# Kernel tuning notes

Hardware: AMD Instinct MI355X
Metric: run time of the kernel (lower is better)

Reference implementation:

```python
import jax, jax.numpy as jnp
import numpy as np
from jax import lax

EPS = 1e-5
T, N, E = 10, 10000, 320000
C_IN, C_HID, C_OUT = 16, 32, 16


def _stgcn_layer(x, edge_index, edge_weight, tw, tb, gw, gb, gamma, beta):
    # x: [T, N, Cin] -> temporal conv over T per node
    xc = jnp.transpose(x, (1, 2, 0))  # [N, Cin, T]
    y = lax.conv_general_dilated(xc, tw, window_strides=(1,), padding=((1, 1),),
                                 dimension_numbers=("NCH", "OIH", "NCH"))
    y = y + tb[None, :, None]
    y = jnp.clip(y, -10.0, 10.0)
    # InstanceNorm1d (affine, biased var over time axis)
    mu = jnp.mean(y, axis=-1, keepdims=True)
    var = jnp.mean((y - mu) ** 2, axis=-1, keepdims=True)
    y = (y - mu) * lax.rsqrt(var + EPS) * gamma[None, :, None] + beta[None, :, None]
    y = jax.nn.relu(y)
    h = jnp.transpose(y, (0, 2, 1))  # [N, T, C]

    n = h.shape[0]
    # GCNConv normalization (identical at every timestep -> computed once)
    ewn = jax.nn.softmax(edge_weight)  # softmax over all E edges
    loop = jnp.arange(n, dtype=edge_index.dtype)
    row = jnp.concatenate([edge_index[0], loop])  # sources (+self loops)
    col = jnp.concatenate([edge_index[1], loop])  # destinations
    w = jnp.concatenate([ewn, jnp.ones((n,), dtype=ewn.dtype)])
    deg = jax.ops.segment_sum(w, col, num_segments=n)
    dinv = jnp.where(deg > 0, lax.rsqrt(jnp.maximum(deg, EPS * 0 + 1e-30)), 0.0)
    norm = dinv[row] * w * dinv[col]  # [E+N]

    hw = jnp.einsum("ntc,cd->ntd", h, gw)  # [N, T, C]
    msg = hw[row] * norm[:, None, None]     # [E+N, T, C] gather
    agg = jax.ops.segment_sum(msg, col, num_segments=n) + gb  # scatter-add
    out = jnp.clip(jax.nn.relu(agg), -10.0, 10.0)
    return jnp.transpose(out, (1, 0, 2))  # [T, N, C]


def setup_inputs() -> dict:
    key = jax.random.key(0)
    ks = jax.random.split(key, 16)
    inp = {
        "x": jax.random.normal(ks[0], (T, N, C_IN), dtype=jnp.float32),
        "edge_index": jax.random.randint(ks[1], (2, E), 0, N, dtype=jnp.int32),
        "edge_weight": jax.random.uniform(ks[2], (E,), dtype=jnp.float32),
        # layer 1 (in -> hid)
        "l1_tw": jax.random.normal(ks[3], (C_HID, C_IN, 3), dtype=jnp.float32) * 0.02,
        "l1_tb": jnp.zeros((C_HID,), dtype=jnp.float32),
        "l1_gw": jax.random.normal(ks[4], (C_HID, C_HID), dtype=jnp.float32) * 0.1,
        "l1_gb": jnp.zeros((C_HID,), dtype=jnp.float32),
        "l1_gamma": jnp.ones((C_HID,), dtype=jnp.float32),
        "l1_beta": jnp.zeros((C_HID,), dtype=jnp.float32),
        # layer 2 (hid -> hid)
        "l2_tw": jax.random.normal(ks[5], (C_HID, C_HID, 3), dtype=jnp.float32) * 0.02,
        "l2_tb": jnp.zeros((C_HID,), dtype=jnp.float32),
        "l2_gw": jax.random.normal(ks[6], (C_HID, C_HID), dtype=jnp.float32) * 0.1,
        "l2_gb": jnp.zeros((C_HID,), dtype=jnp.float32),
        "l2_gamma": jnp.ones((C_HID,), dtype=jnp.float32),
        "l2_beta": jnp.zeros((C_HID,), dtype=jnp.float32),
        # output linear
        "out_w": jax.random.normal(ks[7], (C_HID, C_OUT), dtype=jnp.float32) * 0.1,
        "out_b": jnp.zeros((C_OUT,), dtype=jnp.float32),
    }
    return inp


def reference(x, edge_index, edge_weight,
              l1_tw, l1_tb, l1_gw, l1_gb, l1_gamma, l1_beta,
              l2_tw, l2_tb, l2_gw, l2_gb, l2_gamma, l2_beta,
              out_w, out_b):
    h = _stgcn_layer(x, edge_index, edge_weight, l1_tw, l1_tb, l1_gw, l1_gb, l1_gamma, l1_beta)
    h = _stgcn_layer(h, edge_index, edge_weight, l2_tw, l2_tb, l2_gw, l2_gb, l2_gamma, l2_beta)
    # per-timestep linear then mean over time == mean then linear, done faithfully
    outs = jnp.einsum("tnc,cd->tnd", h, out_w) + out_b
    return jnp.mean(outs, axis=0)  # [N, C_OUT]
```

## Files before the change

kernel.cpp:

```cpp
#include <hip/hip_runtime.h>
#include <hip/hip_bf16.h>
#include <string.h>


typedef __hip_bfloat16 bf16;

#define TSTEPS 10
#define TPAD 12
#define CHID 32
#define ROWELE (TSTEPS * CHID)
#define ROWW4 40

__device__ __forceinline__ float b2f(bf16 v) { return __bfloat162float(v); }
__device__ __forceinline__ float ldf(const void* p, long i, int bf) {
    return bf ? __bfloat162float(((const bf16*)p)[i]) : ((const float*)p)[i];
}
__device__ __forceinline__ int detect_bf(const unsigned* gbits) {
    return (gbits[0] != 0x3F800000u) ? 1 : 0;
}
__device__ __forceinline__ float bflo(unsigned u) { return __uint_as_float(u << 16); }
__device__ __forceinline__ float bfhi(unsigned u) { return __uint_as_float(u & 0xFFFF0000u); }
__device__ __forceinline__ unsigned pack2bf(float a, float b) {
    bf16 x = __float2bfloat16(a), y = __float2bfloat16(b);
    unsigned short ux, uy;
    memcpy(&ux, &x, 2); memcpy(&uy, &y, 2);
    return (unsigned)ux | ((unsigned)uy << 16);
}
__device__ __forceinline__ unsigned short bfbits(float a) {
    bf16 x = __float2bfloat16(a);
    unsigned short u; memcpy(&u, &x, 2);
    return u;
}
__device__ __forceinline__ void accum8(float* f, uint4 u, float w) {
    f[0] += w * bflo(u.x); f[1] += w * bfhi(u.x);
    f[2] += w * bflo(u.y); f[3] += w * bfhi(u.y);
    f[4] += w * bflo(u.z); f[5] += w * bfhi(u.z);
    f[6] += w * bflo(u.w); f[7] += w * bfhi(u.w);
}


__global__ __launch_bounds__(256) void edge_pass_kernel(
    const void* __restrict__ ew, const unsigned* __restrict__ gbits,
    const int* __restrict__ ei,
    float* __restrict__ ewn, float* __restrict__ degx, int* __restrict__ cnt,
    float* sumexp, int E) {
    int bf = detect_bf(gbits);
    int i0 = (blockIdx.x * 256 + threadIdx.x) * 4;
    float e0 = 0.0f, e1 = 0.0f, e2 = 0.0f, e3 = 0.0f;
    if ((E & 3) == 0 && i0 + 3 < E) {
        float w0, w1, w2, w3;
        if (bf) {
            uint2 u = ((const uint2*)ew)[i0 >> 2];
            w0 = bflo(u.x); w1 = bfhi(u.x); w2 = bflo(u.y); w3 = bfhi(u.y);
        } else {
            float4 f = ((const float4*)ew)[i0 >> 2];
            w0 = f.x; w1 = f.y; w2 = f.z; w3 = f.w;
        }
        e0 = __expf(w0); e1 = __expf(w1); e2 = __expf(w2); e3 = __expf(w3);
        int4 c4 = *(const int4*)&ei[E + i0];
        atomicAdd(&degx[c4.x], e0); atomicAdd(&cnt[c4.x], 1);
        atomicAdd(&degx[c4.y], e1); atomicAdd(&cnt[c4.y], 1);
        atomicAdd(&degx[c4.z], e2); atomicAdd(&cnt[c4.z], 1);
        atomicAdd(&degx[c4.w], e3); atomicAdd(&cnt[c4.w], 1);
        *(float4*)&ewn[i0] = make_float4(e0, e1, e2, e3);
    } else {
        float es[4] = {0, 0, 0, 0};
        for (int j = 0; j < 4; j++) {
            int i = i0 + j;
            if (i < E) {
                float e = __expf(ldf(ew, i, bf));
                es[j] = e;
                ewn[i] = e;
                int c = ei[E + i];
                atomicAdd(&degx[c], e);
                atomicAdd(&cnt[c], 1);
            }
        }
        e0 = es[0]; e1 = es[1]; e2 = es[2]; e3 = es[3];
    }
    float v = (e0 + e1) + (e2 + e3);
    for (int o = 32; o > 0; o >>= 1) v += __shfl_down(v, o);
    __shared__ float s[4];
    int lane = threadIdx.x & 63, wv = threadIdx.x >> 6;
    if (lane == 0) s[wv] = v;
    __syncthreads();
    if (threadIdx.x == 0) atomicAdd(sumexp, s[0] + s[1] + s[2] + s[3]);
}

__global__ __launch_bounds__(1024) void scan_kernel(const int* __restrict__ cnt,
                                                    const float* __restrict__ degx,
                                                    const float* __restrict__ sumexp,
                                                    float* __restrict__ dinv,
                                                    int* __restrict__ off, int N) {
    __shared__ int s[1024];
    int tid = threadIdx.x;
    float invS = 1.0f / (*sumexp);
    for (int i = tid; i < N; i += 1024) dinv[i] = rsqrtf(1.0f + degx[i] * invS);
    int chunk = (N + 1023) / 1024;
    int b0 = tid * chunk;
    int p = 0;
    for (int k = 0; k < chunk; k++) { int i = b0 + k; if (i < N) p += cnt[i]; }
    s[tid] = p;
    __syncthreads();
    for (int d = 1; d < 1024; d <<= 1) {
        int v = (tid >= d) ? s[tid - d] : 0;
        __syncthreads();
        s[tid] += v;
        __syncthreads();
    }
    int base = s[tid] - p;
    for (int k = 0; k < chunk; k++) {
        int i = b0 + k;
        if (i < N) {
            off[i] = base;
            base += cnt[i];
            if (i == N - 1) off[N] = base;
        }
    }
}


__global__ __launch_bounds__(256) void fill_kernel(const int* __restrict__ ei,
                                                   const float* __restrict__ ewn,
                                                   const float* __restrict__ dinv,
                                                   const float* __restrict__ sumexp,
                                                   const int* __restrict__ off,
                                                   int* __restrict__ cursor,
                                                   int2* __restrict__ csr, int E) {
    int i0 = (blockIdx.x * 256 + threadIdx.x) * 4;
    if (i0 >= E) return;
    float invS = 1.0f / (*sumexp);
    if ((E & 3) == 0 && i0 + 3 < E) {
        int4 r4 = *(const int4*)&ei[i0];
        int4 c4 = *(const int4*)&ei[E + i0];
        float4 e4 = *(const float4*)&ewn[i0];
        int rr[4] = {r4.x, r4.y, r4.z, r4.w};
        int cc[4] = {c4.x, c4.y, c4.z, c4.w};
        float ee[4] = {e4.x, e4.y, e4.z, e4.w};
#pragma unroll
        for (int j = 0; j < 4; j++) {
            int r = rr[j], c = cc[j];
            int p = atomicAdd(&cursor[c], 1);
            float w = dinv[r] * (ee[j] * invS) * dinv[c];
            csr[off[c] + p] = make_int2(r, __float_as_int(w));
        }
    } else {
        for (int j = 0; j < 4; j++) {
            int i = i0 + j;
            if (i >= E) break;
            int r = ei[i], c = ei[E + i];
            int p = atomicAdd(&cursor[c], 1);
            float w = dinv[r] * (ewn[i] * invS) * dinv[c];
            csr[off[c] + p] = make_int2(r, __float_as_int(w));
        }
    }
}


template <int CIN, int LAYOUT>
__global__ __launch_bounds__(256) void conv_kernel(
    const void* __restrict__ in_, const unsigned* __restrict__ gbits,
    const void* __restrict__ tw, const void* __restrict__ tb,
    const void* __restrict__ gamma, const void* __restrict__ beta,
    const void* __restrict__ gw,
    bf16* __restrict__ hw, int N) {
    constexpr int CO = CHID;
    __shared__ __align__(16) float s_in[8 * CIN * TPAD];
    __shared__ __align__(16) float s_h[8 * CO * TPAD];
    __shared__ __align__(16) unsigned s_tw01[CIN * CO];
    __shared__ __align__(16) unsigned short s_tw2[CIN * CO];
    __shared__ __align__(16) unsigned s_gwp[(CO / 2) * CO];

    int bfw = detect_bf(gbits);
    int tid = threadIdx.x;
    int nl = tid >> 5, o = tid & 31;

    float tbv = ldf(tb, o, bfw);
    float gav = ldf(gamma, o, bfw);
    float bev = ldf(beta, o, bfw);

    for (int i = tid; i < CIN * CO; i += 256) {
        int ci = i / CO, oo = i % CO;
        long base = ((long)oo * CIN + ci) * 3;
        float w0 = ldf(tw, base, bfw);
        float w1 = ldf(tw, base + 1, bfw);
        float w2 = ldf(tw, base + 2, bfw);
        s_tw01[ci * CO + oo] = pack2bf(w0, w1);
        s_tw2[ci * CO + oo] = bfbits(w2);
    }
    for (int i = tid; i < (CO / 2) * CO; i += 256) {
        int cp = i / CO, oo = i % CO;
        s_gwp[i] = pack2bf(ldf(gw, (long)(2 * cp) * CO + oo, bfw),
                           ldf(gw, (long)(2 * cp + 1) * CO + oo, bfw));
    }

    int nb = blockIdx.x * 8;

    if (LAYOUT == 0) {
        constexpr int CP = CIN / 2;
        for (int i2 = tid; i2 < 8 * TSTEPS * CP; i2 += 256) {
            int cp = i2 % CP;
            int t = (i2 / CP) % TSTEPS;
            int nn = i2 / (CP * TSTEPS);
            int n = nb + nn;
            float v0 = 0.0f, v1 = 0.0f;
            if (n < N) {
                long idx = (long)t * ((long)N * CIN) + (long)n * CIN + 2 * cp;
                if (bfw) {
                    unsigned u = ((const unsigned*)in_)[idx >> 1];
                    v0 = bflo(u); v1 = bfhi(u);
                } else {
                    float2 f = ((const float2*)in_)[idx >> 1];
                    v0 = f.x; v1 = f.y;
                }
            }
            int b = nn * (CIN * TPAD) + (2 * cp) * TPAD + t;
            s_in[b] = v0;
            s_in[b + TPAD] = v1;
        }
    } else {
        for (int i2 = tid; i2 < 8 * CIN * 5; i2 += 256) {
            int tp = i2 % 5;
            int ci = (i2 / 5) % CIN;
            int nn = i2 / (5 * CIN);
            int n = nb + nn;
            float v0 = 0.0f, v1 = 0.0f;
            if (n < N) {
                long idx = (long)n * (CIN * TSTEPS) + ci * TSTEPS + 2 * tp;
                unsigned u = ((const unsigned*)in_)[idx >> 1];
                v0 = bflo(u); v1 = bfhi(u);
            }
            int b = nn * (CIN * TPAD) + ci * TPAD + 2 * tp;
            s_in[b] = v0;
            s_in[b + 1] = v1;
        }
    }
    __syncthreads();

    int n = nb + nl;
    const float* xrow = &s_in[nl * CIN * TPAD];

    float acc[TSTEPS];
#pragma unroll
    for (int t = 0; t < TSTEPS; t++) acc[t] = tbv;

    for (int ci = 0; ci < CIN; ci++) {
        const float4* xp = (const float4*)&xrow[ci * TPAD];
        float4 A = xp[0], B = xp[1], C = xp[2];
        float xr[TSTEPS] = {A.x, A.y, A.z, A.w, B.x, B.y, B.z, B.w, C.x, C.y};
        unsigned w01 = s_tw01[ci * CO + o];
        float w0 = bflo(w01), w1 = bfhi(w01);
        float w2 = __uint_as_float(((unsigned)s_tw2[ci * CO + o]) << 16);
        acc[0] += xr[0] * w1 + xr[1] * w2;
#pragma unroll
        for (int t = 1; t < TSTEPS - 1; t++)
            acc[t] += xr[t - 1] * w0 + xr[t] * w1 + xr[t + 1] * w2;
        acc[TSTEPS - 1] += xr[TSTEPS - 2] * w0 + xr[TSTEPS - 1] * w1;
    }

#pragma unroll
    for (int t = 0; t < TSTEPS; t++) acc[t] = fminf(fmaxf(acc[t], -10.0f), 10.0f);
    float mu = 0.0f;
#pragma unroll
    for (int t = 0; t < TSTEPS; t++) mu += acc[t];
    mu *= 0.1f;
    float var = 0.0f;
#pragma unroll
    for (int t = 0; t < TSTEPS; t++) { float d = acc[t] - mu; var += d * d; }
    var *= 0.1f;
    float sc = gav * rsqrtf(var + 1e-5f);
    float h[TSTEPS];
#pragma unroll
    for (int t = 0; t < TSTEPS; t++) h[t] = fmaxf((acc[t] - mu) * sc + bev, 0.0f);

    float4* hp = (float4*)&s_h[nl * CO * TPAD + o * TPAD];
    hp[0] = make_float4(h[0], h[1], h[2], h[3]);
    hp[1] = make_float4(h[4], h[5], h[6], h[7]);
    hp[2] = make_float4(h[8], h[9], 0.0f, 0.0f);
    __syncthreads();

    float acc2[TSTEPS];
#pragma unroll
    for (int t = 0; t < TSTEPS; t++) acc2[t] = 0.0f;
    const float* hrow = &s_h[nl * CO * TPAD];
    for (int cp = 0; cp < CO / 2; cp++) {
        unsigned g2 = s_gwp[cp * CO + o];
        float g0 = bflo(g2), g1 = bfhi(g2);
        const float4* r0 = (const float4*)&hrow[(2 * cp) * TPAD];
        const float4* r1 = (const float4*)&hrow[(2 * cp + 1) * TPAD];
        float4 A0 = r0[0], B0 = r0[1], C0 = r0[2];
        float4 A1 = r1[0], B1 = r1[1], C1 = r1[2];
        acc2[0] += A0.x * g0 + A1.x * g1;
        acc2[1] += A0.y * g0 + A1.y * g1;
        acc2[2] += A0.z * g0 + A1.z * g1;
        acc2[3] += A0.w * g0 + A1.w * g1;
        acc2[4] += B0.x * g0 + B1.x * g1;
        acc2[5] += B0.y * g0 + B1.y * g1;
        acc2[6] += B0.z * g0 + B1.z * g1;
        acc2[7] += B0.w * g0 + B1.w * g1;
        acc2[8] += C0.x * g0 + C1.x * g1;
        acc2[9] += C0.y * g0 + C1.y * g1;
    }
    if (n < N) {
        unsigned* hwp = (unsigned*)hw;
        long base = (long)n * (ROWELE / 2) + o * (TSTEPS / 2);
#pragma unroll
        for (int j = 0; j < 5; j++)
            hwp[base + j] = pack2bf(acc2[2 * j], acc2[2 * j + 1]);
    }
}


template <bool FINAL>
__global__ __launch_bounds__(320) void agg_kernel_t(
    const uint4* __restrict__ hw4, const int* __restrict__ off,
    const int2* __restrict__ csr,
    const float* __restrict__ dinv, const void* __restrict__ gb,
    const void* __restrict__ ow, const void* __restrict__ ob,
    const unsigned* __restrict__ gbits,
    void* __restrict__ out, int N) {
    __shared__ int2 s_sw[ROWELE];
    __shared__ float s_part[8 * ROWW4 * 9];
    __shared__ float s_hbar[CHID];
    __shared__ float s_ow[CHID * 16];
    __shared__ float s_ob[16];

    int bf = detect_bf(gbits);
    int n = blockIdx.x;
    int tid = threadIdx.x;
    int g = tid % ROWW4;
    int eo = tid / ROWW4;

    if (FINAL) {
        for (int i = tid; i < CHID * 16; i += ROWELE) s_ow[i] = ldf(ow, i, bf);
        if (tid < 16) s_ob[tid] = ldf(ob, tid, bf);
    }

    float facc[8];
#pragma unroll
    for (int j = 0; j < 8; j++) facc[j] = 0.0f;

    float dn = dinv[n];
    if (eo == 0) {
        uint4 u = hw4[n * ROWW4 + g];
        accum8(facc, u, dn * dn);
    }

    int beg = off[n], end = off[n + 1];
    for (int base = beg; base < end; base += ROWELE) {
        int m = min(ROWELE, end - base);
        if (tid < m) s_sw[tid] = csr[base + tid];
        __syncthreads();
        int kmax = (m + 7) >> 3;
        int k = 0;
        for (; k + 2 <= kmax; k += 2) {
            int j0 = (k << 3) + eo, j1 = j0 + 8;
            int c0 = min(j0, m - 1), c1 = min(j1, m - 1);
            int2 e0 = s_sw[c0], e1 = s_sw[c1];
            float w0 = (j0 < m) ? __int_as_float(e0.y) : 0.0f;
            float w1 = (j1 < m) ? __int_as_float(e1.y) : 0.0f;
            uint4 u0 = hw4[e0.x * ROWW4 + g];
            uint4 u1 = hw4[e1.x * ROWW4 + g];
            accum8(facc, u0, w0);
            accum8(facc, u1, w1);
        }
        if (k < kmax) {
            int j0 = (k << 3) + eo;
            int c0 = min(j0, m - 1);
            int2 e0 = s_sw[c0];
            float w0 = (j0 < m) ? __int_as_float(e0.y) : 0.0f;
            uint4 u0 = hw4[e0.x * ROWW4 + g];
            accum8(facc, u0, w0);
        }
        __syncthreads();
    }

    {
        float* rowp = &s_part[(eo * ROWW4 + g) * 9];
#pragma unroll
        for (int j = 0; j < 8; j++) rowp[j] = facc[j];
    }
    __syncthreads();
    int gg = tid >> 3, jj = tid & 7;
    float v = 0.0f;
#pragma unroll
    for (int s = 0; s < 8; s++) v += s_part[(s * ROWW4 + gg) * 9 + jj];
    int c = tid / TSTEPS;
    v += ldf(gb, c, bf);
    v = fminf(fmaxf(v, 0.0f), 10.0f);

    if (!FINAL) {
        ((bf16*)out)[(long)n * ROWELE + tid] = __float2bfloat16(v);
    } else {
        __syncthreads();
        s_part[tid] = v;
        __syncthreads();
        if (tid < CHID) {
            float s = 0.0f;
#pragma unroll
            for (int t = 0; t < TSTEPS; t++) s += s_part[tid * TSTEPS + t];
            s_hbar[tid] = s * 0.1f;
        }
        __syncthreads();
        if (tid < 16) {
            float a = s_ob[tid];
#pragma unroll
            for (int cc = 0; cc < CHID; cc++) a += s_hbar[cc] * s_ow[cc * 16 + tid];
            long oi = (long)n * 16 + tid;
            if (bf) ((bf16*)out)[oi] = __float2bfloat16(a);
            else    ((float*)out)[oi] = a;
        }
    }
}


extern "C" void kernel_launch(void* const* d_in, const int* in_sizes, int n_in,
                              void* d_out, int out_size, void* d_ws, size_t ws_size,
                              hipStream_t stream) {
    (void)n_in; (void)out_size; (void)ws_size;

    const void* x     = d_in[0];
    const int*  ei    = (const int*)d_in[1];
    const void* ew    = d_in[2];
    const void* l1_tw = d_in[3];
    const void* l1_tb = d_in[4];
    const void* l1_gw = d_in[5];
    const void* l1_gb = d_in[6];
    const unsigned* gbits = (const unsigned*)d_in[7];
    const void* l1_ga = d_in[7];
    const void* l1_be = d_in[8];
    const void* l2_tw = d_in[9];
    const void* l2_tb = d_in[10];
    const void* l2_gw = d_in[11];
    const void* l2_gb = d_in[12];
    const void* l2_ga = d_in[13];
    const void* l2_be = d_in[14];
    const void* out_w = d_in[15];
    const void* out_b = d_in[16];

    const int N = in_sizes[0] / (TSTEPS * 16);
    const int E = in_sizes[1] / 2;

    char* p = (char*)d_ws;
    auto alloc = [&](size_t bytes) -> char* {
        char* r = p;
        p += (bytes + 255) & ~(size_t)255;
        return r;
    };
    char* zbase   = p;
    float* sumexp = (float*)alloc(256);
    float* degx   = (float*)alloc((size_t)N * 4);
    int*   cnt    = (int*)alloc((size_t)N * 4);
    int*   cursor = (int*)alloc((size_t)N * 4);
    size_t zbytes = (size_t)(p - zbase);
    float* ewn     = (float*)alloc((size_t)E * 4);
    float* dinv    = (float*)alloc((size_t)N * 4);
    int*   offA    = (int*)alloc((size_t)(N + 1) * 4);
    int2*  csr     = (int2*)alloc((size_t)E * 8);
    bf16*  bufA    = (bf16*)alloc((size_t)N * ROWELE * 2);
    bf16*  bufB    = (bf16*)alloc((size_t)N * ROWELE * 2);

    int gE4 = (E + 1023) / 1024;
    int gConv = (N + 7) / 8;

    hipMemsetAsync(zbase, 0, zbytes, stream);
    hipLaunchKernelGGL(edge_pass_kernel, dim3(gE4), dim3(256), 0, stream,
                       ew, gbits, ei, ewn, degx, cnt, sumexp, E);
    hipLaunchKernelGGL(scan_kernel, dim3(1), dim3(1024), 0, stream,
                       cnt, degx, sumexp, dinv, offA, N);
    hipLaunchKernelGGL(fill_kernel, dim3(gE4), dim3(256), 0, stream,
                       ei, ewn, dinv, sumexp, offA, cursor, csr, E);

    hipLaunchKernelGGL((conv_kernel<16, 0>), dim3(gConv), dim3(256), 0, stream,
                       x, gbits, l1_tw, l1_tb, l1_ga, l1_be, l1_gw, bufA, N);
    hipLaunchKernelGGL((agg_kernel_t<false>), dim3(N), dim3(ROWELE), 0, stream,
                       (const uint4*)bufA, offA, csr, dinv, l1_gb,
                       nullptr, nullptr, gbits, (void*)bufB, N);
    hipLaunchKernelGGL((conv_kernel<32, 1>), dim3(gConv), dim3(256), 0, stream,
                       (const void*)bufB, gbits, l2_tw, l2_tb, l2_ga, l2_be, l2_gw, bufA, N);
    hipLaunchKernelGGL((agg_kernel_t<true>), dim3(N), dim3(ROWELE), 0, stream,
                       (const uint4*)bufA, offA, csr, dinv, l2_gb,
                       out_w, out_b, gbits, d_out, N);
}
```

Measured before the change: 287.7 us.

## Fuse graph preprocessing into one cooperative kernel with grid syncs

The memset, edge pass, single-block scan and CSR fill are merged into one cooperative kernel that uses grid-wide syncs between phases. The scan becomes two-level, with per-thread partials combined by one block. The stored exp(edge weight) buffer is dropped and exp is recomputed in the fill phase. This removes several launches and the serial 1024-thread scan block, but adds grid-sync overhead and caps the grid at 2048 blocks, which must all be co-resident.

```diff
diff --git a/kernel.cpp b/kernel.cpp
--- a/kernel.cpp
+++ b/kernel.cpp
@@ -1,7 +1,10 @@
 #include <hip/hip_runtime.h>
 #include <hip/hip_bf16.h>
+#include <hip/hip_cooperative_groups.h>
 #include <string.h>
 
+
+namespace cg = cooperative_groups;
 
 typedef __hip_bfloat16 bf16;
 
@@ -37,121 +40,134 @@
     f[4] += w * bflo(u.z); f[5] += w * bfhi(u.z);
     f[6] += w * bflo(u.w); f[7] += w * bfhi(u.w);
 }
-
-
-__global__ __launch_bounds__(256) void edge_pass_kernel(
+__device__ __forceinline__ void load_ew4(const void* ew, long i0, int bf,
+                                         float& w0, float& w1, float& w2, float& w3) {
+    if (bf) {
+        uint2 u = ((const uint2*)ew)[i0 >> 2];
+        w0 = bflo(u.x); w1 = bfhi(u.x); w2 = bflo(u.y); w3 = bfhi(u.y);
+    } else {
+        float4 f = ((const float4*)ew)[i0 >> 2];
+        w0 = f.x; w1 = f.y; w2 = f.z; w3 = f.w;
+    }
+}
+
+
+__global__ __launch_bounds__(256) void prep_kernel(
     const void* __restrict__ ew, const unsigned* __restrict__ gbits,
     const int* __restrict__ ei,
-    float* __restrict__ ewn, float* __restrict__ degx, int* __restrict__ cnt,
-    float* sumexp, int E) {
-    int bf = detect_bf(gbits);
-    int i0 = (blockIdx.x * 256 + threadIdx.x) * 4;
-    float e0 = 0.0f, e1 = 0.0f, e2 = 0.0f, e3 = 0.0f;
-    if ((E & 3) == 0 && i0 + 3 < E) {
-        float w0, w1, w2, w3;
-        if (bf) {
-            uint2 u = ((const uint2*)ew)[i0 >> 2];
-            w0 = bflo(u.x); w1 = bfhi(u.x); w2 = bflo(u.y); w3 = bfhi(u.y);
+    float* __restrict__ degx, int* __restrict__ cnt, int* __restrict__ cursor,
+    float* __restrict__ sumexp, int* __restrict__ partials,
+    float* __restrict__ dinv, int* __restrict__ off,
+    int2* __restrict__ csr, int N, int E) {
+    cg::grid_group grid = cg::this_grid();
+    const int bf = detect_bf(gbits);
+    const int tid = threadIdx.x;
+    const int gtid = blockIdx.x * 256 + tid;
+    const int gsize = gridDim.x * 256;
+
+    for (int i = gtid; i < N; i += gsize) { degx[i] = 0.0f; cnt[i] = 0; cursor[i] = 0; }
+    if (gtid == 0) *sumexp = 0.0f;
+    grid.sync();
+
+    float esum = 0.0f;
+    for (long i0 = (long)gtid * 4; i0 < E; i0 += (long)gsize * 4) {
+        if ((E & 3) == 0 && i0 + 3 < E) {
+            float w0, w1, w2, w3;
+            load_ew4(ew, i0, bf, w0, w1, w2, w3);
+            float e0 = __expf(w0), e1 = __expf(w1), e2 = __expf(w2), e3 = __expf(w3);
+            int4 c4 = *(const int4*)&ei[E + i0];
+            atomicAdd(&degx[c4.x], e0); atomicAdd(&cnt[c4.x], 1);
+            atomicAdd(&degx[c4.y], e1); atomicAdd(&cnt[c4.y], 1);
+            atomicAdd(&degx[c4.z], e2); atomicAdd(&cnt[c4.z], 1);
+            atomicAdd(&degx[c4.w], e3); atomicAdd(&cnt[c4.w], 1);
+            esum += (e0 + e1) + (e2 + e3);
         } else {
-            float4 f = ((const float4*)ew)[i0 >> 2];
-            w0 = f.x; w1 = f.y; w2 = f.z; w3 = f.w;
-        }
-        e0 = __expf(w0); e1 = __expf(w1); e2 = __expf(w2); e3 = __expf(w3);
-        int4 c4 = *(const int4*)&ei[E + i0];
-        atomicAdd(&degx[c4.x], e0); atomicAdd(&cnt[c4.x], 1);
-        atomicAdd(&degx[c4.y], e1); atomicAdd(&cnt[c4.y], 1);
-        atomicAdd(&degx[c4.z], e2); atomicAdd(&cnt[c4.z], 1);
-        atomicAdd(&degx[c4.w], e3); atomicAdd(&cnt[c4.w], 1);
-        *(float4*)&ewn[i0] = make_float4(e0, e1, e2, e3);
-    } else {
-        float es[4] = {0, 0, 0, 0};
-        for (int j = 0; j < 4; j++) {
-            int i = i0 + j;
-            if (i < E) {
-                float e = __expf(ldf(ew, i, bf));
-                es[j] = e;
-                ewn[i] = e;
-                int c = ei[E + i];
-                atomicAdd(&degx[c], e);
-                atomicAdd(&cnt[c], 1);
+            for (int j = 0; j < 4; j++) {
+                long i = i0 + j;
+                if (i < E) {
+                    float e = __expf(ldf(ew, i, bf));
+                    int c = ei[E + i];
+                    atomicAdd(&degx[c], e);
+                    atomicAdd(&cnt[c], 1);
+                    esum += e;
+                }
             }
         }
-        e0 = es[0]; e1 = es[1]; e2 = es[2]; e3 = es[3];
-    }
-    float v = (e0 + e1) + (e2 + e3);
-    for (int o = 32; o > 0; o >>= 1) v += __shfl_down(v, o);
-    __shared__ float s[4];
-    int lane = threadIdx.x & 63, wv = threadIdx.x >> 6;
-    if (lane == 0) s[wv] = v;
-    __syncthreads();
-    if (threadIdx.x == 0) atomicAdd(sumexp, s[0] + s[1] + s[2] + s[3]);
-}
-
-__global__ __launch_bounds__(1024) void scan_kernel(const int* __restrict__ cnt,
-                                                    const float* __restrict__ degx,
-                                                    const float* __restrict__ sumexp,
-                                                    float* __restrict__ dinv,
-                                                    int* __restrict__ off, int N) {
-    __shared__ int s[1024];
-    int tid = threadIdx.x;
-    float invS = 1.0f / (*sumexp);
-    for (int i = tid; i < N; i += 1024) dinv[i] = rsqrtf(1.0f + degx[i] * invS);
-    int chunk = (N + 1023) / 1024;
-    int b0 = tid * chunk;
-    int p = 0;
-    for (int k = 0; k < chunk; k++) { int i = b0 + k; if (i < N) p += cnt[i]; }
-    s[tid] = p;
-    __syncthreads();
-    for (int d = 1; d < 1024; d <<= 1) {
-        int v = (tid >= d) ? s[tid - d] : 0;
+    }
+    for (int o = 32; o > 0; o >>= 1) esum += __shfl_down(esum, o);
+    if ((tid & 63) == 0 && esum != 0.0f) atomicAdd(sumexp, esum);
+    grid.sync();
+
+    const float invS = 1.0f / (*sumexp);
+
+    for (int i = gtid; i < N; i += gsize) dinv[i] = rsqrtf(1.0f + degx[i] * invS);
+    const int chunk = (N + 1023) >> 10;
+    if (gtid < 1024) {
+        int b0 = gtid * chunk, p = 0;
+        for (int k = 0; k < chunk; k++) { int i = b0 + k; if (i < N) p += cnt[i]; }
+        partials[gtid] = p;
+    }
+    grid.sync();
+
+    if (blockIdx.x == 0) {
+        __shared__ int ss[256];
+        int4 v = ((const int4*)partials)[tid];
+        int loc = v.x + v.y + v.z + v.w;
+        ss[tid] = loc;
         __syncthreads();
-        s[tid] += v;
-        __syncthreads();
-    }
-    int base = s[tid] - p;
-    for (int k = 0; k < chunk; k++) {
-        int i = b0 + k;
-        if (i < N) {
-            off[i] = base;
-            base += cnt[i];
-            if (i == N - 1) off[N] = base;
-        }
-    }
-}
-
-
-__global__ __launch_bounds__(256) void fill_kernel(const int* __restrict__ ei,
-                                                   const float* __restrict__ ewn,
-                                                   const float* __restrict__ dinv,
-                                                   const float* __restrict__ sumexp,
-                                                   const int* __restrict__ off,
-                                                   int* __restrict__ cursor,
-                                                   int2* __restrict__ csr, int E) {
-    int i0 = (blockIdx.x * 256 + threadIdx.x) * 4;
-    if (i0 >= E) return;
-    float invS = 1.0f / (*sumexp);
-    if ((E & 3) == 0 && i0 + 3 < E) {
-        int4 r4 = *(const int4*)&ei[i0];
-        int4 c4 = *(const int4*)&ei[E + i0];
-        float4 e4 = *(const float4*)&ewn[i0];
-        int rr[4] = {r4.x, r4.y, r4.z, r4.w};
-        int cc[4] = {c4.x, c4.y, c4.z, c4.w};
-        float ee[4] = {e4.x, e4.y, e4.z, e4.w};
-#pragma unroll
-        for (int j = 0; j < 4; j++) {
-            int r = rr[j], c = cc[j];
-            int p = atomicAdd(&cursor[c], 1);
-            float w = dinv[r] * (ee[j] * invS) * dinv[c];
-            csr[off[c] + p] = make_int2(r, __float_as_int(w));
-        }
-    } else {
-        for (int j = 0; j < 4; j++) {
-            int i = i0 + j;
-            if (i >= E) break;
-            int r = ei[i], c = ei[E + i];
-            int p = atomicAdd(&cursor[c], 1);
-            float w = dinv[r] * (ewn[i] * invS) * dinv[c];
-            csr[off[c] + p] = make_int2(r, __float_as_int(w));
+        for (int d = 1; d < 256; d <<= 1) {
+            int u = (tid >= d) ? ss[tid - d] : 0;
+            __syncthreads();
+            ss[tid] += u;
+            __syncthreads();
+        }
+        int eb = ss[tid] - loc;
+        ((int4*)partials)[tid] =
+            make_int4(eb, eb + v.x, eb + v.x + v.y, eb + v.x + v.y + v.z);
+    }
+    grid.sync();
+
+    if (gtid < 1024) {
+        int b0 = gtid * chunk;
+        int base = partials[gtid];
+        for (int k = 0; k < chunk; k++) {
+            int i = b0 + k;
+            if (i < N) {
+                off[i] = base;
+                base += cnt[i];
+                if (i == N - 1) off[N] = base;
+            }
+        }
+    }
+    grid.sync();
+
+    for (long i0 = (long)gtid * 4; i0 < E; i0 += (long)gsize * 4) {
+        if ((E & 3) == 0 && i0 + 3 < E) {
+            float w0, w1, w2, w3;
+            load_ew4(ew, i0, bf, w0, w1, w2, w3);
+            float ee[4] = {__expf(w0), __expf(w1), __expf(w2), __expf(w3)};
+            int4 r4 = *(const int4*)&ei[i0];
+            int4 c4 = *(const int4*)&ei[E + i0];
+            int rr[4] = {r4.x, r4.y, r4.z, r4.w};
+            int cc[4] = {c4.x, c4.y, c4.z, c4.w};
+#pragma unroll
+            for (int j = 0; j < 4; j++) {
+                int r = rr[j], c = cc[j];
+                int p = atomicAdd(&cursor[c], 1);
+                float w = dinv[r] * (ee[j] * invS) * dinv[c];
+                csr[off[c] + p] = make_int2(r, __float_as_int(w));
+            }
+        } else {
+            for (int j = 0; j < 4; j++) {
+                long i = i0 + j;
+                if (i < E) {
+                    float e = __expf(ldf(ew, i, bf));
+                    int r = ei[i], c = ei[E + i];
+                    int p = atomicAdd(&cursor[c], 1);
+                    float w = dinv[r] * (e * invS) * dinv[c];
+                    csr[off[c] + p] = make_int2(r, __float_as_int(w));
+                }
+            }
         }
     }
 }
@@ -438,8 +454,8 @@
     const void* out_w = d_in[15];
     const void* out_b = d_in[16];
 
-    const int N = in_sizes[0] / (TSTEPS * 16);
-    const int E = in_sizes[1] / 2;
+    int N = in_sizes[0] / (TSTEPS * 16);
+    int E = in_sizes[1] / 2;
 
     char* p = (char*)d_ws;
     auto alloc = [&](size_t bytes) -> char* {
@@ -447,30 +463,30 @@
         p += (bytes + 255) & ~(size_t)255;
         return r;
     };
-    char* zbase   = p;
-    float* sumexp = (float*)alloc(256);
-    float* degx   = (float*)alloc((size_t)N * 4);
-    int*   cnt    = (int*)alloc((size_t)N * 4);
-    int*   cursor = (int*)alloc((size_t)N * 4);
-    size_t zbytes = (size_t)(p - zbase);
-    float* ewn     = (float*)alloc((size_t)E * 4);
-    float* dinv    = (float*)alloc((size_t)N * 4);
-    int*   offA    = (int*)alloc((size_t)(N + 1) * 4);
-    int2*  csr     = (int2*)alloc((size_t)E * 8);
-    bf16*  bufA    = (bf16*)alloc((size_t)N * ROWELE * 2);
-    bf16*  bufB    = (bf16*)alloc((size_t)N * ROWELE * 2);
-
-    int gE4 = (E + 1023) / 1024;
+    float* sumexp   = (float*)alloc(256);
+    float* degx     = (float*)alloc((size_t)N * 4);
+    int*   cnt      = (int*)alloc((size_t)N * 4);
+    int*   cursor   = (int*)alloc((size_t)N * 4);
+    int*   partials = (int*)alloc(1024 * 4);
+    float* dinv     = (float*)alloc((size_t)N * 4);
+    int*   offA     = (int*)alloc((size_t)(N + 1) * 4);
+    int2*  csr      = (int2*)alloc((size_t)E * 8);
+    bf16*  bufA     = (bf16*)alloc((size_t)N * ROWELE * 2);
+    bf16*  bufB     = (bf16*)alloc((size_t)N * ROWELE * 2);
+
+    int G = (int)((((long)E + 3) / 4 + 255) / 256);
+    if (G < 4) G = 4;
+    if (G > 2048) G = 2048;
+    void* args[] = {
+        (void*)&ew, (void*)&gbits, (void*)&ei,
+        (void*)&degx, (void*)&cnt, (void*)&cursor,
+        (void*)&sumexp, (void*)&partials, (void*)&dinv, (void*)&offA,
+        (void*)&csr, (void*)&N, (void*)&E
+    };
+    hipLaunchCooperativeKernel((const void*)prep_kernel, dim3(G), dim3(256),
+                               args, 0, stream);
+
     int gConv = (N + 7) / 8;
-
-    hipMemsetAsync(zbase, 0, zbytes, stream);
-    hipLaunchKernelGGL(edge_pass_kernel, dim3(gE4), dim3(256), 0, stream,
-                       ew, gbits, ei, ewn, degx, cnt, sumexp, E);
-    hipLaunchKernelGGL(scan_kernel, dim3(1), dim3(1024), 0, stream,
-                       cnt, degx, sumexp, dinv, offA, N);
-    hipLaunchKernelGGL(fill_kernel, dim3(gE4), dim3(256), 0, stream,
-                       ei, ewn, dinv, sumexp, offA, cursor, csr, E);
-
     hipLaunchKernelGGL((conv_kernel<16, 0>), dim3(gConv), dim3(256), 0, stream,
                        x, gbits, l1_tw, l1_tb, l1_ga, l1_be, l1_gw, bufA, N);
     hipLaunchKernelGGL((agg_kernel_t<false>), dim3(N), dim3(ROWELE), 0, stream,
```

Measured after the change: 462.2 us. 60.7% more time.
